# Optimization experiments

Measured on AMD Instinct MI355X. Metric: run time of the kernel, lower is better.

## Reference

```python
import jax, jax.numpy as jnp
import numpy as np

B, N, C = 8, 4096, 1024
H, D = 16, 64
FF = 4096
EPS_ATTN = 1e-6
EPS_LN = 1e-5


def layer_norm(x, g, b, eps=EPS_LN):
    mu = jnp.mean(x, axis=-1, keepdims=True)
    var = jnp.mean(jnp.square(x - mu), axis=-1, keepdims=True)
    return (x - mu) * jax.lax.rsqrt(var + eps) * g + b


def phi(x):
    # elu(x) + 1
    return jnp.where(x > 0, x + 1.0, jnp.exp(x))


def setup_inputs() -> dict:
    key = jax.random.key(0)
    ks = jax.random.split(key, 8)
    src = jax.random.normal(ks[0], (B, N, C), dtype=jnp.float32)
    lengths = jax.random.randint(ks[1], (B,), int(0.75 * N), N + 1)
    src_key_padding_mask = jnp.arange(N)[None, :] >= lengths[:, None]
    s = 0.02
    qkv_w = jax.random.normal(ks[2], (3 * C, C), dtype=jnp.float32) * s
    qkv_b = jnp.zeros((3 * C,), jnp.float32)
    out_w = jax.random.normal(ks[3], (C, C), dtype=jnp.float32) * s
    out_b = jnp.zeros((C,), jnp.float32)
    w1 = jax.random.normal(ks[4], (FF, C), dtype=jnp.float32) * s
    b1 = jnp.zeros((FF,), jnp.float32)
    w2 = jax.random.normal(ks[5], (C, FF), dtype=jnp.float32) * s
    b2 = jnp.zeros((C,), jnp.float32)
    ln1_g = jnp.ones((C,), jnp.float32)
    ln1_b = jnp.zeros((C,), jnp.float32)
    ln2_g = jnp.ones((C,), jnp.float32)
    ln2_b = jnp.zeros((C,), jnp.float32)
    return dict(src=src, src_key_padding_mask=src_key_padding_mask,
                qkv_w=qkv_w, qkv_b=qkv_b, out_w=out_w, out_b=out_b,
                w1=w1, b1=b1, w2=w2, b2=b2,
                ln1_g=ln1_g, ln1_b=ln1_b, ln2_g=ln2_g, ln2_b=ln2_b)


def linear_attention(x, mask, qkv_w, qkv_b, out_w, out_b):
    b, n, c = x.shape
    qkv = (x @ qkv_w.T + qkv_b).reshape(b, n, 3, H, D)
    qkv = jnp.transpose(qkv, (2, 0, 3, 1, 4))  # [3,B,H,N,D]
    q, k, v = qkv[0], qkv[1], qkv[2]
    qf, kf = phi(q), phi(k)
    valid = (~mask).astype(kf.dtype)[:, None, :, None]  # [B,1,N,1]
    kf = kf * valid
    v = v * valid
    kv = jnp.einsum('bhnd,bhne->bhde', kf, v)          # [B,H,D,D]
    z = kf.sum(axis=2)                                  # [B,H,D]
    y_num = jnp.einsum('bhnd,bhde->bhne', qf, kv)       # [B,H,N,D]
    y_den = jnp.maximum(jnp.einsum('bhnd,bhd->bhn', qf, z), EPS_ATTN)
    y = y_num / y_den[..., None]
    y = jnp.transpose(y, (0, 2, 1, 3)).reshape(b, n, c)
    return y @ out_w.T + out_b


def reference(src, src_key_padding_mask, qkv_w, qkv_b, out_w, out_b,
              w1, b1, w2, b2, ln1_g, ln1_b, ln2_g, ln2_b):
    # pre-norm: attention block
    attn_out = linear_attention(layer_norm(src, ln1_g, ln1_b), src_key_padding_mask,
                                qkv_w, qkv_b, out_w, out_b)
    x = src + attn_out
    # pre-norm: FFN block (exact gelu, matching torch F.gelu default)
    h = jax.nn.gelu(layer_norm(x, ln2_g, ln2_b) @ w1.T + b1, approximate=False)
    return x + (h @ w2.T + b2)
```

## Files before the change

### kernel.cpp

```cpp
#include <hip/hip_runtime.h>
#include <cmath>
#include <cstdint>

#define MTOK 32768
#define CDIM 1024
#define SEQ  4096
#define NHEAD 16
#define HDIM 64
#define FFDIM 4096

typedef __attribute__((ext_vector_type(8))) short short8;
typedef __attribute__((ext_vector_type(4))) float f32x4;

static __device__ __forceinline__ float b2f(unsigned short u){
  union { unsigned int i; float f; } c; c.i = ((unsigned int)u)<<16; return c.f;
}
static __device__ __forceinline__ unsigned short f2b(float f){
  union { float f; unsigned int i; } c; c.f = f;
  return (unsigned short)((c.i + 0x7fffu + ((c.i>>16)&1u)) >> 16);
}
static __device__ __forceinline__ void async16(const void* g, void* l){
  __builtin_amdgcn_global_load_lds((const __attribute__((address_space(1))) void*)g,
                                   (__attribute__((address_space(3))) void*)l, 16, 0, 0);
}

__global__ void detect_mask_kernel(const unsigned int* __restrict__ m, int* __restrict__ flag){
  __shared__ int any;
  if(threadIdx.x==0) any=0;
  __syncthreads();
  int loc=0;
  for(int i=threadIdx.x;i<8192;i+=256) if(m[i]>1u) loc=1;
  if(loc) atomicOr(&any,1);
  __syncthreads();
  if(threadIdx.x==0) *flag=any;
}
__global__ void decode_mask_kernel(const void* __restrict__ m, const int* __restrict__ flag,
                                   float* __restrict__ validf){
  int i = blockIdx.x*256 + threadIdx.x;
  int pad = (*flag) ? (int)((const unsigned char*)m)[i] : ((const int*)m)[i];
  validf[i] = pad ? 0.f : 1.f;
}

__global__ void cast_bf16_kernel(const float* __restrict__ x, unsigned short* __restrict__ y, int n){
  int i = (blockIdx.x*256 + threadIdx.x)*4;
  if(i>=n) return;
  float4 v = *(const float4*)(x+i);
  ushort4 o; o.x=f2b(v.x); o.y=f2b(v.y); o.z=f2b(v.z); o.w=f2b(v.w);
  *(ushort4*)(y+i)=o;
}

__global__ __launch_bounds__(256) void ln_kernel(const float* __restrict__ x,
    const float* __restrict__ g, const float* __restrict__ bt, unsigned short* __restrict__ out){
  int row = blockIdx.x, t = threadIdx.x;
  const float* xr = x + (size_t)row*CDIM;
  float4 v = *(const float4*)(xr + t*4);
  float s1 = v.x+v.y+v.z+v.w;
  float s2 = v.x*v.x+v.y*v.y+v.z*v.z+v.w*v.w;
  #pragma unroll
  for(int off=32; off>0; off>>=1){ s1+=__shfl_down(s1,off); s2+=__shfl_down(s2,off); }
  __shared__ float a1[4], a2[4];
  __shared__ float mu_s, rs_s;
  if((t&63)==0){ a1[t>>6]=s1; a2[t>>6]=s2; }
  __syncthreads();
  if(t==0){
    float u1=a1[0]+a1[1]+a1[2]+a1[3], u2=a2[0]+a2[1]+a2[2]+a2[3];
    float mu=u1*(1.f/CDIM);
    mu_s=mu; rs_s=rsqrtf(u2*(1.f/CDIM)-mu*mu+1e-5f);
  }
  __syncthreads();
  float mu=mu_s, rs=rs_s;
  float4 gg=*(const float4*)(g+t*4), bb=*(const float4*)(bt+t*4);
  ushort4 o;
  o.x=f2b((v.x-mu)*rs*gg.x+bb.x);
  o.y=f2b((v.y-mu)*rs*gg.y+bb.y);
  o.z=f2b((v.z-mu)*rs*gg.z+bb.z);
  o.w=f2b((v.w-mu)*rs*gg.w+bb.w);
  *(ushort4*)(out+(size_t)row*CDIM+t*4)=o;
}

template<int MODE>
__global__ __launch_bounds__(256,2) void gemm_bt(
    const unsigned short* __restrict__ A, const unsigned short* __restrict__ Bw,
    const float* __restrict__ bias, const float* __restrict__ extra,
    float* __restrict__ Cf, unsigned short* __restrict__ Cb,
    int M, int N, int K)
{
  __shared__ __align__(16) unsigned short As[128*64];
  __shared__ __align__(16) unsigned short Bs[128*64];
  const int tid = threadIdx.x;
  const int wave = tid>>6, lane = tid&63;
  const int wm = wave>>1, wn = wave&1;
  const int f   = blockIdx.y * gridDim.x + blockIdx.x;
  const int xcd = f & 7, kk = f >> 3;
  const int nx  = kk % gridDim.x;
  const int ny  = (kk / gridDim.x) * 8 + xcd;
  const int m0 = ny*128, n0 = nx*128;
  const int lrow = lane>>3;
  const int gcol = (((lane&7) ^ lrow))*8;

  f32x4 acc[4][4];
  #pragma unroll
  for(int i=0;i<4;i++)
    #pragma unroll
    for(int j=0;j<4;j++) acc[i][j]=(f32x4)(0.f);

  const int ar = wm*64 + (lane&15);
  const int br = wn*64 + (lane&15);
  const int kc = lane>>4;
  const int xorv = lane&7;

  for(int kt=0; kt<K; kt+=64){
    #pragma unroll
    for(int it=0; it<4; it++){
      int wo = wave*4+it;
      int r  = wo*8 + lrow;
      async16(A  + (size_t)(m0+r)*K + kt + gcol, (void*)&As[wo*512]);
      async16(Bw + (size_t)(n0+r)*K + kt + gcol, (void*)&Bs[wo*512]);
    }
    __syncthreads();
    #pragma unroll
    for(int ks=0; ks<2; ks++){
      const int ch = ((ks*4 + kc) ^ xorv)*8;
      short8 a[4], b[4];
      #pragma unroll
      for(int i=0;i<4;i++){
        a[i]=*(const short8*)&As[(ar+i*16)*64 + ch];
        b[i]=*(const short8*)&Bs[(br+i*16)*64 + ch];
      }
      #pragma unroll
      for(int i=0;i<4;i++)
        #pragma unroll
        for(int j=0;j<4;j++)
          acc[i][j]=__builtin_amdgcn_mfma_f32_16x16x32_bf16(a[i],b[j],acc[i][j],0,0,0);
    }
    __syncthreads();
  }
  const int rbase = m0 + wm*64 + (lane>>4)*4;
  const int cbase = n0 + wn*64 + (lane&15);
  #pragma unroll
  for(int mi=0;mi<4;mi++){
    #pragma unroll
    for(int i=0;i<4;i++){
      int m = rbase + mi*16 + i;
      #pragma unroll
      for(int ni=0;ni<4;ni++){
        int n = cbase + ni*16;
        float v = acc[mi][ni][i] + bias[n];
        if(MODE==0){
          float valid = extra[m];
          int part = n>>10;
          float p = (v>0.f)? (v+1.f) : __expf(v);
          float r = (part==0)? p : (part==1? p*valid : v*valid);
          Cb[(size_t)m*N + n] = f2b(r);
        } else if(MODE==1){
          size_t off=(size_t)m*N+n;
          Cf[off] = v + extra[off];
        } else if(MODE==2){
          float gl = 0.5f*v*(1.f+erff(v*0.70710678118654752f));
          Cb[(size_t)m*N+n] = f2b(gl);
        } else {
          size_t off=(size_t)m*N+n;
          Cf[off] += v;
        }
      }
    }
  }
}

__global__ __launch_bounds__(256) void kvz_partial_kernel(
    const unsigned short* __restrict__ qkv, float* __restrict__ kvp, float* __restrict__ zp)
{
  const int chunk = blockIdx.x;
  const int bh = blockIdx.y;
  const int b = bh>>4, h = bh&15;
  const int t = threadIdx.x;
  __shared__ float kfs[16][64];
  __shared__ float vs[16][64];
  float acc[4][4]={{0}}; float zacc[4]={0};
  const int td=t&15, te=t>>4;
  const int d0=td*4, e0=te*4;
  const int lr=t>>4, lc=(t&15)*4;
  for(int s=0;s<16;s++){
    size_t m  = (size_t)(b*SEQ + chunk*256 + s*16 + lr);
    size_t rb = m*3072 + (size_t)h*64;
    ushort4 k4 = *(const ushort4*)(qkv + rb + 1024 + lc);
    ushort4 v4 = *(const ushort4*)(qkv + rb + 2048 + lc);
    __syncthreads();
    kfs[lr][lc]=b2f(k4.x); kfs[lr][lc+1]=b2f(k4.y); kfs[lr][lc+2]=b2f(k4.z); kfs[lr][lc+3]=b2f(k4.w);
    vs [lr][lc]=b2f(v4.x); vs [lr][lc+1]=b2f(v4.y); vs [lr][lc+2]=b2f(v4.z); vs [lr][lc+3]=b2f(v4.w);
    __syncthreads();
    #pragma unroll
    for(int n=0;n<16;n++){
      float4 kq=*(const float4*)&kfs[n][d0];
      float4 vv=*(const float4*)&vs[n][e0];
      float kqa[4]={kq.x,kq.y,kq.z,kq.w};
      float vva[4]={vv.x,vv.y,vv.z,vv.w};
      #pragma unroll
      for(int i=0;i<4;i++)
        #pragma unroll
        for(int j=0;j<4;j++) acc[i][j]+=kqa[i]*vva[j];
      if(te==0){ zacc[0]+=kq.x; zacc[1]+=kq.y; zacc[2]+=kq.z; zacc[3]+=kq.w; }
    }
  }
  const int pidx = bh*16 + chunk;
  float* kvd = kvp + (size_t)pidx*4096;
  #pragma unroll
  for(int i=0;i<4;i++){
    float4 o={acc[i][0],acc[i][1],acc[i][2],acc[i][3]};
    *(float4*)(kvd + (d0+i)*64 + e0)=o;
  }
  if(te==0){
    float4 o={zacc[0],zacc[1],zacc[2],zacc[3]};
    *(float4*)(zp + (size_t)pidx*64 + d0)=o;
  }
}

__global__ void kvz_reduce_kernel(const float* __restrict__ kvp, const float* __restrict__ zp,
                                  float* __restrict__ kv, float* __restrict__ z){
  int bh = blockIdx.x, t = threadIdx.x;
  for(int j=t; j<4096; j+=256){
    float s=0;
    for(int c=0;c<16;c++) s += kvp[((size_t)bh*16+c)*4096 + j];
    kv[(size_t)bh*4096 + j] = s;
  }
  if(t<64){
    float s=0;
    for(int c=0;c<16;c++) s += zp[((size_t)bh*16+c)*64 + t];
    z[bh*64+t]=s;
  }
}

__global__ __launch_bounds__(256) void y_kernel(
    const unsigned short* __restrict__ qkv, const float* __restrict__ kv,
    const float* __restrict__ z, unsigned short* __restrict__ ybuf)
{
  const int nch = blockIdx.x;
  const int bh  = blockIdx.y;
  const int b = bh>>4, h = bh&15;
  const int t = threadIdx.x;
  __shared__ float kvs[64][64];
  __shared__ float qfs[64][68];
  __shared__ float zs[64];
  for(int j=t*4; j<4096; j+=1024){
    float4 vv=*(const float4*)(kv+(size_t)bh*4096+j);
    ((float*)kvs)[j]=vv.x; ((float*)kvs)[j+1]=vv.y; ((float*)kvs)[j+2]=vv.z; ((float*)kvs)[j+3]=vv.w;
  }
  if(t<64) zs[t]=z[bh*64+t];
  for(int s=0;s<4;s++){
    int row=s*16+(t>>4), col=(t&15)*4;
    size_t m=(size_t)(b*SEQ+nch*64+row);
    ushort4 q4=*(const ushort4*)(qkv+m*3072+(size_t)h*64+col);
    qfs[row][col]=b2f(q4.x); qfs[row][col+1]=b2f(q4.y); qfs[row][col+2]=b2f(q4.z); qfs[row][col+3]=b2f(q4.w);
  }
  __syncthreads();
  const int tn=t>>4, te=t&15;
  const int nr0=tn*4, e0=te*4;
  float acc[4][4]={{0}}; float den[4]={0};
  #pragma unroll 4
  for(int d=0;d<64;d++){
    float4 kv4=*(const float4*)&kvs[d][e0];
    float zd=zs[d];
    #pragma unroll
    for(int i=0;i<4;i++){
      float q=qfs[nr0+i][d];
      acc[i][0]+=q*kv4.x; acc[i][1]+=q*kv4.y; acc[i][2]+=q*kv4.z; acc[i][3]+=q*kv4.w;
      den[i]+=q*zd;
    }
  }
  #pragma unroll
  for(int i=0;i<4;i++){
    float inv=1.f/fmaxf(den[i],1e-6f);
    ushort4 o;
    o.x=f2b(acc[i][0]*inv); o.y=f2b(acc[i][1]*inv); o.z=f2b(acc[i][2]*inv); o.w=f2b(acc[i][3]*inv);
    size_t m=(size_t)(b*SEQ+nch*64+nr0+i);
    *(ushort4*)(ybuf+m*1024+(size_t)h*64+e0)=o;
  }
}

extern "C" void kernel_launch(void* const* d_in, const int* in_sizes, int n_in,
                              void* d_out, int out_size, void* d_ws, size_t ws_size,
                              hipStream_t stream)
{
  const float* src   = (const float*)d_in[0];
  const void*  mask  = d_in[1];
  const float* qkv_w = (const float*)d_in[2];
  const float* qkv_b = (const float*)d_in[3];
  const float* out_w = (const float*)d_in[4];
  const float* out_b = (const float*)d_in[5];
  const float* w1    = (const float*)d_in[6];
  const float* b1    = (const float*)d_in[7];
  const float* w2    = (const float*)d_in[8];
  const float* b2    = (const float*)d_in[9];
  const float* ln1g  = (const float*)d_in[10];
  const float* ln1b  = (const float*)d_in[11];
  const float* ln2g  = (const float*)d_in[12];
  const float* ln2b  = (const float*)d_in[13];
  float* out = (float*)d_out;
  char* ws = (char*)d_ws;

  size_t o = 0;
  int* flag = (int*)(ws);                         o += 256;
  float* validf = (float*)(ws+o);                 o += (size_t)MTOK*4;
  unsigned short* wqb = (unsigned short*)(ws+o);  o += (size_t)3072*1024*2;
  unsigned short* wob = (unsigned short*)(ws+o);  o += (size_t)1024*1024*2;
  unsigned short* w1b = (unsigned short*)(ws+o);  o += (size_t)4096*1024*2;
  unsigned short* w2b = (unsigned short*)(ws+o);  o += (size_t)1024*4096*2;
  unsigned short* bufA = (unsigned short*)(ws+o); o += (size_t)MTOK*1024*2;
  char* R = ws+o;                                 o += (size_t)MTOK*4096*2;
  unsigned short* qkvbuf = (unsigned short*)R;
  float* kvp = (float*)(R + (size_t)MTOK*3072*2);
  float* zp  = (float*)(R + (size_t)MTOK*3072*2 + (size_t)2048*4096*4);
  unsigned short* hbuf = (unsigned short*)R;
  float* kv = (float*)(ws+o);                     o += (size_t)128*4096*4;
  float* zv = (float*)(ws+o);                     o += (size_t)128*64*4;

  detect_mask_kernel<<<1,256,0,stream>>>((const unsigned int*)mask, flag);
  decode_mask_kernel<<<MTOK/256,256,0,stream>>>(mask, flag, validf);
  cast_bf16_kernel<<<3072,256,0,stream>>>(qkv_w, wqb, 3072*1024);
  cast_bf16_kernel<<<1024,256,0,stream>>>(out_w, wob, 1024*1024);
  cast_bf16_kernel<<<4096,256,0,stream>>>(w1,  w1b, 4096*1024);
  cast_bf16_kernel<<<8192,256,0,stream>>>(w2,  w2b, 1024*4096);

  ln_kernel<<<MTOK,256,0,stream>>>(src, ln1g, ln1b, bufA);
  gemm_bt<0><<<dim3(3072/128, MTOK/128),256,0,stream>>>(bufA, wqb, qkv_b, validf, nullptr, qkvbuf, MTOK,3072,1024);
  kvz_partial_kernel<<<dim3(16,128),256,0,stream>>>(qkvbuf, kvp, zp);
  kvz_reduce_kernel<<<128,256,0,stream>>>(kvp, zp, kv, zv);
  y_kernel<<<dim3(64,128),256,0,stream>>>(qkvbuf, kv, zv, bufA);
  gemm_bt<1><<<dim3(1024/128, MTOK/128),256,0,stream>>>(bufA, wob, out_b, src, out, nullptr, MTOK,1024,1024);
  ln_kernel<<<MTOK,256,0,stream>>>(out, ln2g, ln2b, bufA);
  gemm_bt<2><<<dim3(4096/128, MTOK/128),256,0,stream>>>(bufA, w1b, b1, nullptr, nullptr, hbuf, MTOK,4096,1024);
  gemm_bt<3><<<dim3(1024/128, MTOK/128),256,0,stream>>>(hbuf, w2b, b2, nullptr, out, nullptr, MTOK,1024,4096);
}
```

Before: 1.471 ms.

## Merge weight casts, use nontemporal GEMM stores, widen kvz staging tile

Fuses the four weight cast launches into one kernel that picks its source by index range. Switches the scalar bf16 and fp32 epilogue stores in the QKV, FFN1 and FFN2 GEMMs to nontemporal stores so the large outputs bypass cache retention. Enlarges the kv partial kernel's shared-memory staging from 16 to 64 rows per sync, cutting barriers while raising LDS use. Nontemporal stores may hurt when the next kernel rereads the data, such as qkvbuf or hbuf.

After: 1.467 ms. About the same (-0.3%).

```diff
diff --git a/kernel.cpp b/kernel.cpp
--- a/kernel.cpp
+++ b/kernel.cpp
@@ -19,6 +19,12 @@
   union { float f; unsigned int i; } c; c.f = f;
   return (unsigned short)((c.i + 0x7fffu + ((c.i>>16)&1u)) >> 16);
 }
+static __device__ __forceinline__ void nt_store_us(unsigned short v, unsigned short* p){
+  __builtin_nontemporal_store(v, p);
+}
+static __device__ __forceinline__ void nt_store_f(float v, float* p){
+  __builtin_nontemporal_store(v, p);
+}
 static __device__ __forceinline__ void async16(const void* g, void* l){
   __builtin_amdgcn_global_load_lds((const __attribute__((address_space(1))) void*)g,
                                    (__attribute__((address_space(3))) void*)l, 16, 0, 0);
@@ -41,12 +47,19 @@
   validf[i] = pad ? 0.f : 1.f;
 }
 
-__global__ void cast_bf16_kernel(const float* __restrict__ x, unsigned short* __restrict__ y, int n){
-  int i = (blockIdx.x*256 + threadIdx.x)*4;
-  if(i>=n) return;
-  float4 v = *(const float4*)(x+i);
+__global__ void cast_all_kernel(const float* __restrict__ a, const float* __restrict__ b,
+                                const float* __restrict__ c, const float* __restrict__ d,
+                                unsigned short* __restrict__ oa, unsigned short* __restrict__ ob,
+                                unsigned short* __restrict__ oc, unsigned short* __restrict__ od){
+  long i = ((long)blockIdx.x*256 + threadIdx.x)*4;
+  const float* x; unsigned short* y; long off;
+  if(i < 3145728){ x=a; y=oa; off=i; }
+  else if(i < 4194304){ x=b; y=ob; off=i-3145728; }
+  else if(i < 8388608){ x=c; y=oc; off=i-4194304; }
+  else { x=d; y=od; off=i-8388608; }
+  float4 v = *(const float4*)(x+off);
   ushort4 o; o.x=f2b(v.x); o.y=f2b(v.y); o.z=f2b(v.z); o.w=f2b(v.w);
-  *(ushort4*)(y+i)=o;
+  *(ushort4*)(y+off)=o;
 }
 
 __global__ __launch_bounds__(256) void ln_kernel(const float* __restrict__ x,
@@ -151,16 +164,16 @@
           int part = n>>10;
           float p = (v>0.f)? (v+1.f) : __expf(v);
           float r = (part==0)? p : (part==1? p*valid : v*valid);
-          Cb[(size_t)m*N + n] = f2b(r);
+          nt_store_us(f2b(r), &Cb[(size_t)m*N + n]);
         } else if(MODE==1){
           size_t off=(size_t)m*N+n;
           Cf[off] = v + extra[off];
         } else if(MODE==2){
           float gl = 0.5f*v*(1.f+erff(v*0.70710678118654752f));
-          Cb[(size_t)m*N+n] = f2b(gl);
+          nt_store_us(f2b(gl), &Cb[(size_t)m*N+n]);
         } else {
           size_t off=(size_t)m*N+n;
-          Cf[off] += v;
+          nt_store_f(Cf[off] + v, &Cf[off]);
         }
       }
     }
@@ -174,23 +187,27 @@
   const int bh = blockIdx.y;
   const int b = bh>>4, h = bh&15;
   const int t = threadIdx.x;
-  __shared__ float kfs[16][64];
-  __shared__ float vs[16][64];
+  __shared__ float kfs[64][64];
+  __shared__ float vs[64][64];
   float acc[4][4]={{0}}; float zacc[4]={0};
   const int td=t&15, te=t>>4;
   const int d0=td*4, e0=te*4;
   const int lr=t>>4, lc=(t&15)*4;
-  for(int s=0;s<16;s++){
-    size_t m  = (size_t)(b*SEQ + chunk*256 + s*16 + lr);
-    size_t rb = m*3072 + (size_t)h*64;
-    ushort4 k4 = *(const ushort4*)(qkv + rb + 1024 + lc);
-    ushort4 v4 = *(const ushort4*)(qkv + rb + 2048 + lc);
+  for(int s=0;s<4;s++){
     __syncthreads();
-    kfs[lr][lc]=b2f(k4.x); kfs[lr][lc+1]=b2f(k4.y); kfs[lr][lc+2]=b2f(k4.z); kfs[lr][lc+3]=b2f(k4.w);
-    vs [lr][lc]=b2f(v4.x); vs [lr][lc+1]=b2f(v4.y); vs [lr][lc+2]=b2f(v4.z); vs [lr][lc+3]=b2f(v4.w);
+    #pragma unroll
+    for(int rr=0; rr<4; rr++){
+      int row = rr*16 + lr;
+      size_t m  = (size_t)(b*SEQ + chunk*256 + s*64 + row);
+      size_t rb = m*3072 + (size_t)h*64;
+      ushort4 k4 = *(const ushort4*)(qkv + rb + 1024 + lc);
+      ushort4 v4 = *(const ushort4*)(qkv + rb + 2048 + lc);
+      kfs[row][lc]=b2f(k4.x); kfs[row][lc+1]=b2f(k4.y); kfs[row][lc+2]=b2f(k4.z); kfs[row][lc+3]=b2f(k4.w);
+      vs [row][lc]=b2f(v4.x); vs [row][lc+1]=b2f(v4.y); vs [row][lc+2]=b2f(v4.z); vs [row][lc+3]=b2f(v4.w);
+    }
     __syncthreads();
-    #pragma unroll
-    for(int n=0;n<16;n++){
+    #pragma unroll 8
+    for(int n=0;n<64;n++){
       float4 kq=*(const float4*)&kfs[n][d0];
       float4 vv=*(const float4*)&vs[n][e0];
       float kqa[4]={kq.x,kq.y,kq.z,kq.w};
@@ -316,10 +333,7 @@
 
   detect_mask_kernel<<<1,256,0,stream>>>((const unsigned int*)mask, flag);
   decode_mask_kernel<<<MTOK/256,256,0,stream>>>(mask, flag, validf);
-  cast_bf16_kernel<<<3072,256,0,stream>>>(qkv_w, wqb, 3072*1024);
-  cast_bf16_kernel<<<1024,256,0,stream>>>(out_w, wob, 1024*1024);
-  cast_bf16_kernel<<<4096,256,0,stream>>>(w1,  w1b, 4096*1024);
-  cast_bf16_kernel<<<8192,256,0,stream>>>(w2,  w2b, 1024*4096);
+  cast_all_kernel<<<12288,256,0,stream>>>(qkv_w, out_w, w1, w2, wqb, wob, w1b, w2b);
 
   ln_kernel<<<MTOK,256,0,stream>>>(src, ln1g, ln1b, bufA);
   gemm_bt<0><<<dim3(3072/128, MTOK/128),256,0,stream>>>(bufA, wqb, qkv_b, validf, nullptr, qkvbuf, MTOK,3072,1024);
```
